# Performance work log

Measured on AMD Instinct MI355X. Metric: run time of the kernel, lower is better.

The kernel has to match this reference:

```python
import jax, jax.numpy as jnp
import numpy as np

NUM_HEAD = 16
EMBD_DIM = 2048
LATENT_DIM = 512
ROPE_DIM = 64  # min(rope_dim, head_dim) = 64
HEAD_DIM = EMBD_DIM // NUM_HEAD  # 128
ROPE_HALF = ROPE_DIM // 2
SCALE = (HEAD_DIM + ROPE_DIM) ** -0.5


def setup_inputs() -> dict:
    key = jax.random.key(0)
    ks = jax.random.split(key, 9)
    B, S = 2, 2048
    std = 0.02
    return {
        "x": jax.random.normal(ks[0], (B, S, EMBD_DIM), dtype=jnp.float32),
        "w_ckv": jax.random.normal(ks[1], (EMBD_DIM, LATENT_DIM), dtype=jnp.float32) * std,
        "w_k": jax.random.normal(ks[2], (LATENT_DIM, EMBD_DIM), dtype=jnp.float32) * std,
        "w_v": jax.random.normal(ks[3], (LATENT_DIM, EMBD_DIM), dtype=jnp.float32) * std,
        "w_cq": jax.random.normal(ks[4], (EMBD_DIM, LATENT_DIM), dtype=jnp.float32) * std,
        "w_q": jax.random.normal(ks[5], (LATENT_DIM, EMBD_DIM), dtype=jnp.float32) * std,
        "w_qr": jax.random.normal(ks[6], (LATENT_DIM, NUM_HEAD * ROPE_DIM), dtype=jnp.float32) * std,
        "w_kr": jax.random.normal(ks[7], (EMBD_DIM, ROPE_DIM), dtype=jnp.float32) * std,
        "w_o": jax.random.normal(ks[8], (EMBD_DIM, EMBD_DIM), dtype=jnp.float32) * std,
    }


def _apply_rope(x, S):
    # x: [B, H, S, D] with D >= ROPE_DIM; interleaved even/odd rotation
    inv_freq = 1.0 / (10000.0 ** (jnp.arange(0, ROPE_DIM, 2, dtype=jnp.float32) / ROPE_DIM))
    pos = jnp.arange(S, dtype=jnp.float32)
    freqs = pos[:, None] * inv_freq[None, :]           # [S, ROPE_HALF]
    cos = jnp.cos(freqs)[None, None]                   # [1,1,S,ROPE_HALF]
    sin = jnp.sin(freqs)[None, None]
    x_rope, x_pass = x[..., :ROPE_DIM], x[..., ROPE_DIM:]
    x_even, x_odd = x_rope[..., 0::2], x_rope[..., 1::2]
    r_even = x_even * cos - x_odd * sin
    r_odd = x_even * sin + x_odd * cos
    rotated = jnp.stack([r_even, r_odd], axis=-1).reshape(x_rope.shape)
    return jnp.concatenate([rotated, x_pass], axis=-1) if x_pass.shape[-1] > 0 else rotated


def reference(x, w_ckv, w_k, w_v, w_cq, w_q, w_qr, w_kr, w_o):
    B, S, _ = x.shape
    c_kv = x @ w_ckv                                   # [B,S,latent]
    k_c = (c_kv @ w_k).reshape(B, S, NUM_HEAD, HEAD_DIM).transpose(0, 2, 1, 3)
    v = (c_kv @ w_v).reshape(B, S, NUM_HEAD, HEAD_DIM).transpose(0, 2, 1, 3)
    c_q = x @ w_cq
    q_c = (c_q @ w_q).reshape(B, S, NUM_HEAD, HEAD_DIM).transpose(0, 2, 1, 3)
    q_r = (c_q @ w_qr).reshape(B, S, NUM_HEAD, ROPE_DIM).transpose(0, 2, 1, 3)
    k_r = (x @ w_kr)[:, None, :, :]                    # [B,1,S,rope] shared across heads
    k_r = jnp.broadcast_to(k_r, (B, NUM_HEAD, S, ROPE_DIM))
    q_r = _apply_rope(q_r, S)
    k_r = _apply_rope(k_r, S)
    q = jnp.concatenate([q_c, q_r], axis=-1)           # [B,H,S,head+rope]
    k = jnp.concatenate([k_c, k_r], axis=-1)
    scores = jnp.einsum("bhsd,bhtd->bhst", q, k) * SCALE
    causal = jnp.tril(jnp.ones((S, S), dtype=bool))
    scores = jnp.where(causal[None, None], scores, -jnp.inf)
    attn = jax.nn.softmax(scores, axis=-1)
    out = jnp.einsum("bhst,bhtd->bhsd", attn, v)       # [B,H,S,head]
    out = out.transpose(0, 2, 1, 3).reshape(B, S, EMBD_DIM)
    return out @ w_o
```

## Files before the change

kernel.cpp:

```cpp
#include <hip/hip_runtime.h>


typedef unsigned short u16;
typedef __attribute__((ext_vector_type(8))) short s16x8;
typedef __attribute__((ext_vector_type(4))) float f32x4;
typedef __attribute__((ext_vector_type(8))) __bf16 bf16x8;
typedef __attribute__((ext_vector_type(4))) u16 u16x4;

#define S_LEN 2048
#define NH 16
#define HD 128
#define DQK 192
#define EMB 2048

#define GLOAD_LDS16(g, l)                                                      \
  __builtin_amdgcn_global_load_lds(                                            \
      (const __attribute__((address_space(1))) unsigned int*)(g),              \
      (__attribute__((address_space(3))) unsigned int*)(l), 16, 0, 0)

__device__ __forceinline__ u16 f2b(float f) {
  unsigned u = __builtin_bit_cast(unsigned, f);
  u += 0x7FFFu + ((u >> 16) & 1u);
  return (u16)(u >> 16);
}
__device__ __forceinline__ float b2f(u16 v) {
  unsigned u = ((unsigned)v) << 16;
  return __builtin_bit_cast(float, u);
}
__device__ __forceinline__ bf16x8 ld_bf8(const u16* p) {
  return __builtin_bit_cast(bf16x8, *(const s16x8*)p);
}

__global__ __launch_bounds__(256) void f2b_kernel(const float* __restrict__ in,
                                                  u16* __restrict__ out, int n4) {
  int i = blockIdx.x * 256 + threadIdx.x;
  if (i >= n4) return;
  f32x4 v = *(const f32x4*)(in + (size_t)i * 4);
  u16x4 o = { f2b(v[0]), f2b(v[1]), f2b(v[2]), f2b(v[3]) };
  *(u16x4*)(out + (size_t)i * 4) = o;
}

__global__ __launch_bounds__(256) void transpose_f2b_kernel(const float* __restrict__ in,
                                                            u16* __restrict__ out,
                                                            int K, int N) {
  __shared__ u16 T[64 * 72];
  const int n0 = blockIdx.x * 64, k0 = blockIdx.y * 64;
  const int t = threadIdx.x;
#pragma unroll
  for (int r = 0; r < 4; ++r) {
    int kl = (t >> 4) + r * 16, nl = (t & 15) * 4;
    f32x4 v = *(const f32x4*)(in + (size_t)(k0 + kl) * N + n0 + nl);
#pragma unroll
    for (int j = 0; j < 4; ++j) T[(nl + j) * 72 + kl] = f2b(v[j]);
  }
  __syncthreads();
#pragma unroll
  for (int r = 0; r < 2; ++r) {
    int chunk = t + r * 256, nr = chunk >> 3, kc = (chunk & 7) * 8;
    *(s16x8*)(out + (size_t)(n0 + nr) * K + k0 + kc) = *(const s16x8*)(&T[nr * 72 + kc]);
  }
}

__global__ __launch_bounds__(256) void rope_table_kernel(float* __restrict__ cosT,
                                                         float* __restrict__ sinT) {
  int id = blockIdx.x * 256 + threadIdx.x;
  int s = id >> 5, i = id & 31;
  float inv = exp2f(-(float)i * (13.287712379549449f / 32.0f));
  float ang = (float)s * inv;
  cosT[id] = cosf(ang);
  sinT[id] = sinf(ang);
}

template<int MODE>
__global__ __launch_bounds__(256) void gemm_bt_kernel(const u16* __restrict__ A,
                                                      int lda,
                                                      const u16* __restrict__ BT,
                                                      void* __restrict__ Cout,
                                                      void* __restrict__ Cout2,
                                                      int M, int N, int K,
                                                      float scale) {
  __shared__ __align__(16) u16 As[2][128 * 64];
  __shared__ __align__(16) u16 Bs[2][128 * 64];
  const int t = threadIdx.x;
  const int lane = t & 63, wid = t >> 6;
  const int wr = (wid >> 1) * 64, wc = (wid & 1) * 64;
  const int bm0 = blockIdx.y * 128, bn0 = blockIdx.x * 128;
  const int lr = lane & 15, lg = lane >> 4;

  auto stage = [&](int k0, int buf) {
#pragma unroll
    for (int r = 0; r < 4; ++r) {
      int chunk = t + r * 256;
      int row = chunk >> 3, kcs = (chunk & 7) * 8;
      int kcg = kcs ^ ((row & 7) << 3);
      GLOAD_LDS16(A + (size_t)(bm0 + row) * lda + k0 + kcg, &As[buf][chunk * 8]);
      GLOAD_LDS16(BT + (size_t)(bn0 + row) * K + k0 + kcg, &Bs[buf][chunk * 8]);
    }
  };

  f32x4 acc[4][4] = {};
  const int nt = K >> 6;
  stage(0, 0);
  for (int tk = 0; tk < nt; ++tk) {
    const int cur = tk & 1;
    __syncthreads();
    if (tk + 1 < nt) stage((tk + 1) << 6, cur ^ 1);
#pragma unroll
    for (int kk = 0; kk < 2; ++kk) {
      bf16x8 af[4], bfr[4];
      const int kbase = kk * 32 + lg * 8;
#pragma unroll
      for (int m = 0; m < 4; ++m) {
        int row = wr + m * 16 + lr;
        af[m] = ld_bf8(&As[cur][row * 64 + (kbase ^ ((row & 7) << 3))]);
      }
#pragma unroll
      for (int n = 0; n < 4; ++n) {
        int row = wc + n * 16 + lr;
        bfr[n] = ld_bf8(&Bs[cur][row * 64 + (kbase ^ ((row & 7) << 3))]);
      }
#pragma unroll
      for (int m = 0; m < 4; ++m)
#pragma unroll
        for (int n = 0; n < 4; ++n)
          acc[m][n] = __builtin_amdgcn_mfma_f32_16x16x32_bf16(af[m], bfr[n], acc[m][n], 0, 0, 0);
    }
  }

#pragma unroll
  for (int m = 0; m < 4; ++m)
#pragma unroll
    for (int n = 0; n < 4; ++n)
#pragma unroll
      for (int rg = 0; rg < 4; ++rg) {
        int row = bm0 + wr + m * 16 + lg * 4 + rg;
        int col = bn0 + wc + n * 16 + lr;
        if (col >= N) continue;
        float v = acc[m][n][rg];
        if (MODE == 0) {
          ((u16*)Cout)[(size_t)row * N + col] = f2b(v * scale);
        } else if (MODE == 1) {
          ((float*)Cout)[(size_t)row * N + col] = v * scale;
        } else if (MODE == 4) {
          int bb = row >> 11, s = row & 2047;
          if (col < 2048) {
            int h = col >> 7, d = col & 127;
            ((u16*)Cout)[((size_t)(bb * NH + h) * S_LEN + s) * DQK + d] = f2b(v);
          } else {
            int c2 = col - 2048, h = c2 >> 7, d = c2 & 127;
            ((u16*)Cout2)[((size_t)(bb * NH + h) * HD + d) * S_LEN + s] = f2b(v);
          }
        } else {
          int bb = row >> 11, s = row & 2047;
          if (col < 2048) {
            int h = col >> 7, d = col & 127;
            ((u16*)Cout)[((size_t)(bb * NH + h) * S_LEN + s) * DQK + d] = f2b(v * scale);
          } else {
            ((u16*)Cout2)[(size_t)row * 1024 + (col - 2048)] = f2b(v);
          }
        }
      }
}

__global__ __launch_bounds__(256) void rope_assemble_kernel(const u16* __restrict__ qr,
                                                            const u16* __restrict__ cc,
                                                            const float* __restrict__ cosT,
                                                            const float* __restrict__ sinT,
                                                            u16* __restrict__ Qcat,
                                                            u16* __restrict__ Kcat) {
  int id = blockIdx.x * 256 + threadIdx.x;
  int i = id & 31;
  int s = (id >> 5) & 2047;
  int h = (id >> 16) & 15;
  int b = id >> 20;
  float c = cosT[(s << 5) + i], sn = sinT[(s << 5) + i];
  const float SC = 0.07216878364870323f;

  size_t qbase = ((size_t)b * S_LEN + s) * 1024 + h * 64 + 2 * i;
  float qe = b2f(qr[qbase]), qo = b2f(qr[qbase + 1]);
  size_t obase = ((size_t)(b * NH + h) * S_LEN + s) * DQK + HD + 2 * i;
  Qcat[obase]     = f2b((qe * c - qo * sn) * SC);
  Qcat[obase + 1] = f2b((qe * sn + qo * c) * SC);

  size_t kbase = ((size_t)b * S_LEN + s) * 1088 + 1024 + 2 * i;
  float ke = b2f(cc[kbase]), ko = b2f(cc[kbase + 1]);
  Kcat[obase]     = f2b(ke * c - ko * sn);
  Kcat[obase + 1] = f2b(ke * sn + ko * c);
}

__global__ __launch_bounds__(512, 2) void attn_kernel(const u16* __restrict__ Q,
                                                      const u16* __restrict__ K,
                                                      const u16* __restrict__ VT,
                                                      u16* __restrict__ O) {
  __shared__ u16 Ks[64 * 200];
  __shared__ u16 Vs[128 * 72];
  __shared__ u16 Ps[8 * 16 * 88];
  const int id = blockIdx.x;
  const int p8 = id >> 5, hb = id & 31;
  const int h = hb & 15, b = hb >> 4;
  const int qb = (p8 < 8) ? p8 : 23 - p8;
  const int q0 = qb * 128;
  const int t = threadIdx.x, lane = t & 63, wid = t >> 6;
  const int lr = lane & 15, lg = lane >> 4;
  const size_t qk_head = (size_t)(b * NH + h) * S_LEN * DQK;
  const size_t vt_head = (size_t)(b * NH + h) * HD * S_LEN;

  s16x8 kst[3], vst[2];
  auto gload = [&](int kt) {
#pragma unroll
    for (int r = 0; r < 3; ++r) {
      int chunk = t + r * 512, row = chunk / 24, cc = chunk % 24;
      kst[r] = *(const s16x8*)(K + qk_head + (size_t)(kt * 64 + row) * DQK + cc * 8);
    }
#pragma unroll
    for (int r = 0; r < 2; ++r) {
      int chunk = t + r * 512, d = chunk >> 3, cc = chunk & 7;
      vst[r] = *(const s16x8*)(VT + vt_head + (size_t)d * S_LEN + kt * 64 + cc * 8);
    }
  };
  auto swr = [&]() {
#pragma unroll
    for (int r = 0; r < 3; ++r) {
      int chunk = t + r * 512, row = chunk / 24, cc = chunk % 24;
      *(s16x8*)(&Ks[row * 200 + cc * 8]) = kst[r];
    }
#pragma unroll
    for (int r = 0; r < 2; ++r) {
      int chunk = t + r * 512, d = chunk >> 3, cc = chunk & 7;
      *(s16x8*)(&Vs[d * 72 + cc * 8]) = vst[r];
    }
  };

  bf16x8 qa[6];
  {
    const u16* qrow = Q + qk_head + (size_t)(q0 + wid * 16 + lr) * DQK;
#pragma unroll
    for (int ks = 0; ks < 6; ++ks) qa[ks] = ld_bf8(qrow + ks * 32 + lg * 8);
  }

  f32x4 acc_o[8] = {};
  float m_r[4] = { -INFINITY, -INFINITY, -INFINITY, -INFINITY };
  float l_r[4] = { 0.f, 0.f, 0.f, 0.f };

  const int nt = 2 * qb + 2;
  gload(0);
#pragma unroll 1
  for (int kt = 0; kt < nt; ++kt) {
    __syncthreads();
    swr();
    if (kt + 1 < nt) gload(kt + 1);
    __syncthreads();

    f32x4 sacc[4];
#pragma unroll
    for (int cb = 0; cb < 4; ++cb) {
      f32x4 sv = {};
#pragma unroll
      for (int ks = 0; ks < 6; ++ks) {
        bf16x8 kb = ld_bf8(&Ks[(cb * 16 + lr) * 200 + ks * 32 + lg * 8]);
        sv = __builtin_amdgcn_mfma_f32_16x16x32_bf16(qa[ks], kb, sv, 0, 0, 0);
      }
      sacc[cb] = sv;
    }

    if (kt >= 2 * qb) {
#pragma unroll
      for (int cb = 0; cb < 4; ++cb)
#pragma unroll
        for (int rg = 0; rg < 4; ++rg) {
          int q_g = q0 + wid * 16 + lg * 4 + rg;
          int kv_g = kt * 64 + cb * 16 + lr;
          if (kv_g > q_g) sacc[cb][rg] = -INFINITY;
        }
    }

    float pmax[4];
#pragma unroll
    for (int rg = 0; rg < 4; ++rg)
      pmax[rg] = fmaxf(fmaxf(sacc[0][rg], sacc[1][rg]), fmaxf(sacc[2][rg], sacc[3][rg]));
#pragma unroll
    for (int off = 1; off < 16; off <<= 1)
#pragma unroll
      for (int rg = 0; rg < 4; ++rg)
        pmax[rg] = fmaxf(pmax[rg], __shfl_xor(pmax[rg], off, 64));

    float alpha[4];
#pragma unroll
    for (int rg = 0; rg < 4; ++rg) {
      float mn = fmaxf(m_r[rg], pmax[rg]);
      alpha[rg] = __expf(m_r[rg] - mn);
      m_r[rg] = mn;
      l_r[rg] *= alpha[rg];
    }
#pragma unroll
    for (int vb = 0; vb < 8; ++vb)
#pragma unroll
      for (int rg = 0; rg < 4; ++rg)
        acc_o[vb][rg] *= alpha[rg];

    float psum[4] = { 0.f, 0.f, 0.f, 0.f };
#pragma unroll
    for (int cb = 0; cb < 4; ++cb)
#pragma unroll
      for (int rg = 0; rg < 4; ++rg) {
        float pv = __expf(sacc[cb][rg] - m_r[rg]);
        sacc[cb][rg] = pv;
        psum[rg] += pv;
      }
#pragma unroll
    for (int off = 1; off < 16; off <<= 1)
#pragma unroll
      for (int rg = 0; rg < 4; ++rg)
        psum[rg] += __shfl_xor(psum[rg], off, 64);
#pragma unroll
    for (int rg = 0; rg < 4; ++rg) l_r[rg] += psum[rg];

    u16* psw = &Ps[wid * (16 * 88)];
#pragma unroll
    for (int cb = 0; cb < 4; ++cb)
#pragma unroll
      for (int rg = 0; rg < 4; ++rg)
        psw[(lg * 4 + rg) * 88 + cb * 16 + lr] = f2b(sacc[cb][rg]);

    bf16x8 pa[2];
#pragma unroll
    for (int ks = 0; ks < 2; ++ks) pa[ks] = ld_bf8(&psw[lr * 88 + ks * 32 + lg * 8]);
#pragma unroll
    for (int vb = 0; vb < 8; ++vb) {
#pragma unroll
      for (int ks = 0; ks < 2; ++ks) {
        bf16x8 vv = ld_bf8(&Vs[(vb * 16 + lr) * 72 + ks * 32 + lg * 8]);
        acc_o[vb] = __builtin_amdgcn_mfma_f32_16x16x32_bf16(pa[ks], vv, acc_o[vb], 0, 0, 0);
      }
    }
  }

#pragma unroll
  for (int vb = 0; vb < 8; ++vb)
#pragma unroll
    for (int rg = 0; rg < 4; ++rg) {
      int s_glob = q0 + wid * 16 + lg * 4 + rg;
      int col = vb * 16 + lr;
      O[((size_t)b * S_LEN + s_glob) * EMB + h * HD + col] = f2b(acc_o[vb][rg] / l_r[rg]);
    }
}

extern "C" void kernel_launch(void* const* d_in, const int* in_sizes, int n_in,
                              void* d_out, int out_size, void* d_ws, size_t ws_size,
                              hipStream_t stream) {
  const float* xf    = (const float*)d_in[0];
  const float* wckvf = (const float*)d_in[1];
  const float* wkf   = (const float*)d_in[2];
  const float* wvf   = (const float*)d_in[3];
  const float* wcqf  = (const float*)d_in[4];
  const float* wqf   = (const float*)d_in[5];
  const float* wqrf  = (const float*)d_in[6];
  const float* wkrf  = (const float*)d_in[7];
  const float* wof   = (const float*)d_in[8];
  (void)in_sizes; (void)n_in; (void)out_size; (void)ws_size;

  u16* ws = (u16*)d_ws;
  size_t off = 0;
  auto alloc = [&](size_t n) -> u16* { u16* p = ws + off; off += n; return p; };
  u16* XB     = alloc(8388608);
  u16* WCKV_T = alloc(1048576);
  u16* WCQ_T  = alloc(1048576);
  u16* WKR_T  = alloc(131072);
  u16* WK_T   = alloc(1048576);
  u16* WV_T   = alloc(1048576);
  u16* WQ_T   = alloc(1048576);
  u16* WQR_T  = alloc(524288);
  u16* WO_T   = alloc(4194304);
  u16* CC     = alloc(4456448);
  u16* QR     = alloc(4194304);
  u16* QCAT   = alloc(12582912);
  u16* KCAT   = alloc(12582912);
  u16* VT     = alloc(8388608);
  u16* AOUT   = alloc(8388608);
  float* COS_T = (float*)alloc(131072);
  float* SIN_T = (float*)alloc(131072);
  (void)WCQ_T; (void)WKR_T; (void)WV_T; (void)WQR_T;

  f2b_kernel<<<8192, 256, 0, stream>>>(xf, XB, 2097152);

  transpose_f2b_kernel<<<dim3(8, 32),  256, 0, stream>>>(wckvf, WCKV_T, 2048, 512);
  transpose_f2b_kernel<<<dim3(8, 32),  256, 0, stream>>>(wcqf,  WCQ_T,  2048, 512);
  transpose_f2b_kernel<<<dim3(1, 32),  256, 0, stream>>>(wkrf,  WKR_T,  2048, 64);
  transpose_f2b_kernel<<<dim3(32, 8),  256, 0, stream>>>(wkf,   WK_T,   512, 2048);
  transpose_f2b_kernel<<<dim3(32, 8),  256, 0, stream>>>(wvf,   WV_T,   512, 2048);
  transpose_f2b_kernel<<<dim3(32, 8),  256, 0, stream>>>(wqf,   WQ_T,   512, 2048);
  transpose_f2b_kernel<<<dim3(16, 8),  256, 0, stream>>>(wqrf,  WQR_T,  512, 1024);
  transpose_f2b_kernel<<<dim3(32, 32), 256, 0, stream>>>(wof,   WO_T,   2048, 2048);

  rope_table_kernel<<<256, 256, 0, stream>>>(COS_T, SIN_T);

  const float SC = 0.07216878364870323f;
  gemm_bt_kernel<0><<<dim3(9, 32),  256, 0, stream>>>(XB, 2048, WCKV_T, CC, nullptr,
                                                      4096, 1088, 2048, 1.0f);
  gemm_bt_kernel<4><<<dim3(32, 32), 256, 0, stream>>>(CC, 1088, WK_T, KCAT, VT,
                                                      4096, 4096, 512, 1.0f);
  gemm_bt_kernel<5><<<dim3(24, 32), 256, 0, stream>>>(CC + 512, 1088, WQ_T, QCAT, QR,
                                                      4096, 3072, 512, SC);

  rope_assemble_kernel<<<8192, 256, 0, stream>>>(QR, CC, COS_T, SIN_T, QCAT, KCAT);

  attn_kernel<<<512, 512, 0, stream>>>(QCAT, KCAT, VT, AOUT);

  gemm_bt_kernel<1><<<dim3(16, 32), 256, 0, stream>>>(AOUT, 2048, WO_T, d_out, nullptr,
                                                      4096, 2048, 2048, 1.0f);
}
```

Baseline: 289.4 us.

## Switch attention to 32x32x16 MFMA with 4 waves of 32 query rows

```diff
diff --git a/kernel.cpp b/kernel.cpp
--- a/kernel.cpp
+++ b/kernel.cpp
@@ -4,6 +4,7 @@
 typedef unsigned short u16;
 typedef __attribute__((ext_vector_type(8))) short s16x8;
 typedef __attribute__((ext_vector_type(4))) float f32x4;
+typedef __attribute__((ext_vector_type(16))) float f32x16;
 typedef __attribute__((ext_vector_type(8))) __bf16 bf16x8;
 typedef __attribute__((ext_vector_type(4))) u16 u16x4;
 
@@ -188,60 +189,62 @@
   Kcat[obase + 1] = f2b(ke * sn + ko * c);
 }
 
-__global__ __launch_bounds__(512, 2) void attn_kernel(const u16* __restrict__ Q,
+__global__ __launch_bounds__(256, 2) void attn_kernel(const u16* __restrict__ Q,
                                                       const u16* __restrict__ K,
                                                       const u16* __restrict__ VT,
                                                       u16* __restrict__ O) {
   __shared__ u16 Ks[64 * 200];
   __shared__ u16 Vs[128 * 72];
-  __shared__ u16 Ps[8 * 16 * 88];
+  __shared__ u16 Ps[4 * 32 * 72];
   const int id = blockIdx.x;
   const int p8 = id >> 5, hb = id & 31;
   const int h = hb & 15, b = hb >> 4;
   const int qb = (p8 < 8) ? p8 : 23 - p8;
   const int q0 = qb * 128;
   const int t = threadIdx.x, lane = t & 63, wid = t >> 6;
-  const int lr = lane & 15, lg = lane >> 4;
+  const int lc = lane & 31, hi = lane >> 5;
   const size_t qk_head = (size_t)(b * NH + h) * S_LEN * DQK;
   const size_t vt_head = (size_t)(b * NH + h) * HD * S_LEN;
 
-  s16x8 kst[3], vst[2];
+  s16x8 kst[6], vst[4];
   auto gload = [&](int kt) {
 #pragma unroll
-    for (int r = 0; r < 3; ++r) {
-      int chunk = t + r * 512, row = chunk / 24, cc = chunk % 24;
+    for (int r = 0; r < 6; ++r) {
+      int chunk = t + r * 256, row = chunk / 24, cc = chunk % 24;
       kst[r] = *(const s16x8*)(K + qk_head + (size_t)(kt * 64 + row) * DQK + cc * 8);
     }
 #pragma unroll
-    for (int r = 0; r < 2; ++r) {
-      int chunk = t + r * 512, d = chunk >> 3, cc = chunk & 7;
+    for (int r = 0; r < 4; ++r) {
+      int chunk = t + r * 256, d = chunk >> 3, cc = chunk & 7;
       vst[r] = *(const s16x8*)(VT + vt_head + (size_t)d * S_LEN + kt * 64 + cc * 8);
     }
   };
   auto swr = [&]() {
 #pragma unroll
-    for (int r = 0; r < 3; ++r) {
-      int chunk = t + r * 512, row = chunk / 24, cc = chunk % 24;
+    for (int r = 0; r < 6; ++r) {
+      int chunk = t + r * 256, row = chunk / 24, cc = chunk % 24;
       *(s16x8*)(&Ks[row * 200 + cc * 8]) = kst[r];
     }
 #pragma unroll
-    for (int r = 0; r < 2; ++r) {
-      int chunk = t + r * 512, d = chunk >> 3, cc = chunk & 7;
+    for (int r = 0; r < 4; ++r) {
+      int chunk = t + r * 256, d = chunk >> 3, cc = chunk & 7;
       *(s16x8*)(&Vs[d * 72 + cc * 8]) = vst[r];
     }
   };
 
-  bf16x8 qa[6];
+  bf16x8 qa[12];
   {
-    const u16* qrow = Q + qk_head + (size_t)(q0 + wid * 16 + lr) * DQK;
-#pragma unroll
-    for (int ks = 0; ks < 6; ++ks) qa[ks] = ld_bf8(qrow + ks * 32 + lg * 8);
+    const u16* qrow = Q + qk_head + (size_t)(q0 + wid * 32 + lc) * DQK;
+#pragma unroll
+    for (int ks = 0; ks < 12; ++ks) qa[ks] = ld_bf8(qrow + ks * 16 + hi * 8);
   }
 
-  f32x4 acc_o[8] = {};
-  float m_r[4] = { -INFINITY, -INFINITY, -INFINITY, -INFINITY };
-  float l_r[4] = { 0.f, 0.f, 0.f, 0.f };
-
+  f32x16 acc_o[4] = {};
+  float m_r[16], l_r[16];
+#pragma unroll
+  for (int r = 0; r < 16; ++r) { m_r[r] = -INFINITY; l_r[r] = 0.f; }
+
+  u16* psw = &Ps[wid * (32 * 72)];
   const int nt = 2 * qb + 2;
   gload(0);
 #pragma unroll 1
@@ -251,97 +254,92 @@
     if (kt + 1 < nt) gload(kt + 1);
     __syncthreads();
 
-    f32x4 sacc[4];
-#pragma unroll
-    for (int cb = 0; cb < 4; ++cb) {
-      f32x4 sv = {};
-#pragma unroll
-      for (int ks = 0; ks < 6; ++ks) {
-        bf16x8 kb = ld_bf8(&Ks[(cb * 16 + lr) * 200 + ks * 32 + lg * 8]);
-        sv = __builtin_amdgcn_mfma_f32_16x16x32_bf16(qa[ks], kb, sv, 0, 0, 0);
-      }
-      sacc[cb] = sv;
+    f32x16 sc[2];
+#pragma unroll
+    for (int cb = 0; cb < 2; ++cb) {
+      f32x16 sv = {};
+#pragma unroll
+      for (int ks = 0; ks < 12; ++ks) {
+        bf16x8 kb = ld_bf8(&Ks[(cb * 32 + lc) * 200 + ks * 16 + hi * 8]);
+        sv = __builtin_amdgcn_mfma_f32_32x32x16_bf16(qa[ks], kb, sv, 0, 0, 0);
+      }
+      sc[cb] = sv;
     }
 
     if (kt >= 2 * qb) {
 #pragma unroll
-      for (int cb = 0; cb < 4; ++cb)
-#pragma unroll
-        for (int rg = 0; rg < 4; ++rg) {
-          int q_g = q0 + wid * 16 + lg * 4 + rg;
-          int kv_g = kt * 64 + cb * 16 + lr;
-          if (kv_g > q_g) sacc[cb][rg] = -INFINITY;
+      for (int cb = 0; cb < 2; ++cb)
+#pragma unroll
+        for (int r = 0; r < 16; ++r) {
+          int q_g = q0 + wid * 32 + (r & 3) + 8 * (r >> 2) + 4 * hi;
+          int kv_g = kt * 64 + cb * 32 + lc;
+          if (kv_g > q_g) sc[cb][r] = -INFINITY;
         }
     }
 
-    float pmax[4];
-#pragma unroll
-    for (int rg = 0; rg < 4; ++rg)
-      pmax[rg] = fmaxf(fmaxf(sacc[0][rg], sacc[1][rg]), fmaxf(sacc[2][rg], sacc[3][rg]));
-#pragma unroll
-    for (int off = 1; off < 16; off <<= 1)
-#pragma unroll
-      for (int rg = 0; rg < 4; ++rg)
-        pmax[rg] = fmaxf(pmax[rg], __shfl_xor(pmax[rg], off, 64));
-
-    float alpha[4];
-#pragma unroll
-    for (int rg = 0; rg < 4; ++rg) {
-      float mn = fmaxf(m_r[rg], pmax[rg]);
-      alpha[rg] = __expf(m_r[rg] - mn);
-      m_r[rg] = mn;
-      l_r[rg] *= alpha[rg];
-    }
-#pragma unroll
-    for (int vb = 0; vb < 8; ++vb)
-#pragma unroll
-      for (int rg = 0; rg < 4; ++rg)
-        acc_o[vb][rg] *= alpha[rg];
-
-    float psum[4] = { 0.f, 0.f, 0.f, 0.f };
-#pragma unroll
-    for (int cb = 0; cb < 4; ++cb)
-#pragma unroll
-      for (int rg = 0; rg < 4; ++rg) {
-        float pv = __expf(sacc[cb][rg] - m_r[rg]);
-        sacc[cb][rg] = pv;
-        psum[rg] += pv;
-      }
-#pragma unroll
-    for (int off = 1; off < 16; off <<= 1)
-#pragma unroll
-      for (int rg = 0; rg < 4; ++rg)
-        psum[rg] += __shfl_xor(psum[rg], off, 64);
-#pragma unroll
-    for (int rg = 0; rg < 4; ++rg) l_r[rg] += psum[rg];
-
-    u16* psw = &Ps[wid * (16 * 88)];
-#pragma unroll
-    for (int cb = 0; cb < 4; ++cb)
-#pragma unroll
-      for (int rg = 0; rg < 4; ++rg)
-        psw[(lg * 4 + rg) * 88 + cb * 16 + lr] = f2b(sacc[cb][rg]);
-
-    bf16x8 pa[2];
-#pragma unroll
-    for (int ks = 0; ks < 2; ++ks) pa[ks] = ld_bf8(&psw[lr * 88 + ks * 32 + lg * 8]);
-#pragma unroll
-    for (int vb = 0; vb < 8; ++vb) {
-#pragma unroll
-      for (int ks = 0; ks < 2; ++ks) {
-        bf16x8 vv = ld_bf8(&Vs[(vb * 16 + lr) * 72 + ks * 32 + lg * 8]);
-        acc_o[vb] = __builtin_amdgcn_mfma_f32_16x16x32_bf16(pa[ks], vv, acc_o[vb], 0, 0, 0);
+    float pmax[16];
+#pragma unroll
+    for (int r = 0; r < 16; ++r) pmax[r] = fmaxf(sc[0][r], sc[1][r]);
+#pragma unroll
+    for (int off = 1; off < 32; off <<= 1)
+#pragma unroll
+      for (int r = 0; r < 16; ++r)
+        pmax[r] = fmaxf(pmax[r], __shfl_xor(pmax[r], off, 64));
+
+#pragma unroll
+    for (int r = 0; r < 16; ++r) {
+      float mn = fmaxf(m_r[r], pmax[r]);
+      float alpha = __expf(m_r[r] - mn);
+      m_r[r] = mn;
+      l_r[r] *= alpha;
+#pragma unroll
+      for (int db = 0; db < 4; ++db) acc_o[db][r] *= alpha;
+    }
+
+    float ps[16];
+#pragma unroll
+    for (int r = 0; r < 16; ++r) ps[r] = 0.f;
+#pragma unroll
+    for (int cb = 0; cb < 2; ++cb)
+#pragma unroll
+      for (int r = 0; r < 16; ++r) {
+        float pv = __expf(sc[cb][r] - m_r[r]);
+        ps[r] += pv;
+        int qrow = (r & 3) + 8 * (r >> 2) + 4 * hi;
+        psw[qrow * 72 + cb * 32 + lc] = f2b(pv);
+      }
+#pragma unroll
+    for (int off = 1; off < 32; off <<= 1)
+#pragma unroll
+      for (int r = 0; r < 16; ++r)
+        ps[r] += __shfl_xor(ps[r], off, 64);
+#pragma unroll
+    for (int r = 0; r < 16; ++r) l_r[r] += ps[r];
+
+    bf16x8 pa[4];
+#pragma unroll
+    for (int ks = 0; ks < 4; ++ks)
+      pa[ks] = ld_bf8(&psw[lc * 72 + ks * 16 + hi * 8]);
+#pragma unroll
+    for (int db = 0; db < 4; ++db) {
+#pragma unroll
+      for (int ks = 0; ks < 4; ++ks) {
+        bf16x8 vb = ld_bf8(&Vs[(db * 32 + lc) * 72 + ks * 16 + hi * 8]);
+        acc_o[db] = __builtin_amdgcn_mfma_f32_32x32x16_bf16(pa[ks], vb, acc_o[db], 0, 0, 0);
       }
     }
   }
 
-#pragma unroll
-  for (int vb = 0; vb < 8; ++vb)
-#pragma unroll
-    for (int rg = 0; rg < 4; ++rg) {
-      int s_glob = q0 + wid * 16 + lg * 4 + rg;
-      int col = vb * 16 + lr;
-      O[((size_t)b * S_LEN + s_glob) * EMB + h * HD + col] = f2b(acc_o[vb][rg] / l_r[rg]);
+  float rl[16];
+#pragma unroll
+  for (int r = 0; r < 16; ++r) rl[r] = 1.0f / l_r[r];
+#pragma unroll
+  for (int db = 0; db < 4; ++db)
+#pragma unroll
+    for (int r = 0; r < 16; ++r) {
+      int s_glob = q0 + wid * 32 + (r & 3) + 8 * (r >> 2) + 4 * hi;
+      int col = db * 32 + lc;
+      O[((size_t)b * S_LEN + s_glob) * EMB + h * HD + col] = f2b(acc_o[db][r] * rl[r]);
     }
 }
 
@@ -404,7 +402,7 @@
 
   rope_assemble_kernel<<<8192, 256, 0, stream>>>(QR, CC, COS_T, SIN_T, QCAT, KCAT);
 
-  attn_kernel<<<512, 512, 0, stream>>>(QCAT, KCAT, VT, AOUT);
+  attn_kernel<<<512, 256, 0, stream>>>(QCAT, KCAT, VT, AOUT);
 
   gemm_bt_kernel<1><<<dim3(16, 32), 256, 0, stream>>>(AOUT, 2048, WO_T, d_out, nullptr,
                                                       4096, 2048, 2048, 1.0f);
```

After: 476.2 us. +64.5%, slower.
